# Optimization experiments

Hardware: AMD Instinct MI355X
Metric: run time of the kernel (lower is better)

The kernel has to match this reference:

```python
import jax, jax.numpy as jnp
import numpy as np

NUM_EMBEDDINGS = 4096
CODE_DIM = 256
NUM_CODEBOOKS = 4
COMMITMENT_COST = 0.25
CODEBOOK_COST = 1.0
EPS = 1e-10


def setup_inputs() -> dict:
    key = jax.random.key(0)
    k1, k2 = jax.random.split(key)
    z_bt = jax.random.normal(k1, (8192, NUM_CODEBOOKS * CODE_DIM), dtype=jnp.float32)
    # codebook init: uniform(-1/K, 1/K) as in the torch module
    embed = jax.random.uniform(k2, (NUM_EMBEDDINGS, CODE_DIM), dtype=jnp.float32,
                               minval=-1.0 / NUM_EMBEDDINGS, maxval=1.0 / NUM_EMBEDDINGS)
    return {"z_bt": z_bt, "embed": embed}


def reference(z_bt, embed):
    K, D = embed.shape            # [num_embeddings, code_dim]
    flat_z = z_bt.reshape(-1, D)  # [N*num_codebooks, code_dim]
    # squared-distance matrix: ||z||^2 - 2 z.e + ||e||^2
    distances = (jnp.sum(flat_z * flat_z, axis=1, keepdims=True)
                 - 2.0 * (flat_z @ embed.T)
                 + jnp.sum(embed * embed, axis=1)[None, :])  # [M, K]
    flat_indices = jnp.argmin(distances, axis=1)              # [M]
    quantized_bt = embed[flat_indices].reshape(z_bt.shape)    # [N, latent_dim]

    # use_ema=True, eval mode: codebook_loss is zero, no EMA buffer update
    codebook_loss = jnp.zeros((), dtype=z_bt.dtype)
    commitment_loss = jnp.mean((jax.lax.stop_gradient(quantized_bt) - z_bt) ** 2)
    loss = CODEBOOK_COST * codebook_loss + COMMITMENT_COST * commitment_loss

    # straight-through estimator
    quantized_st = z_bt + jax.lax.stop_gradient(quantized_bt - z_bt)

    # perplexity via histogram (same math as one_hot.mean(0))
    M = flat_indices.shape[0]
    counts = jnp.zeros((K,), dtype=z_bt.dtype).at[flat_indices].add(1.0)
    avg_probs = counts / M
    perplexity = jnp.exp(-jnp.sum(avg_probs * jnp.log(avg_probs + EPS)))

    indices = flat_indices.reshape(-1, NUM_CODEBOOKS)
    return quantized_st, indices, loss, codebook_loss, commitment_loss, perplexity
```

## Files before the change

kernel.cpp:

```cpp
#include <hip/hip_runtime.h>


constexpr int D_CODE  = 256;
constexpr int M_ROWS  = 32768;
constexpr int K_EMB   = 4096;
constexpr long Q_ELEMS = 8388608L;

constexpr size_t OFF_SUMZ = 0;
constexpr size_t OFF_SUME = 131072;
constexpr size_t OFF_PART = 147456;
constexpr size_t OFF_IDX  = 1196032;
constexpr size_t OFF_HIST = 1327104;
constexpr size_t OFF_DACC = 1343488;
constexpr size_t ZERO_LEN = 16392;

__device__ __forceinline__ float comp4(const float4& v, int kr) {
  return kr == 0 ? v.x : (kr == 1 ? v.y : (kr == 2 ? v.z : v.w));
}
__device__ __forceinline__ unsigned long long umin64(unsigned long long a, unsigned long long b) {
  return a < b ? a : b;
}

__global__ __launch_bounds__(256) void k_rowsums(const float* __restrict__ z,
                                                 const float* __restrict__ emb,
                                                 float* __restrict__ sumz,
                                                 float* __restrict__ sume) {
  int w = threadIdx.x >> 6, lane = threadIdx.x & 63;
  int row = blockIdx.x * 4 + w;
  const float* src;
  float* dst;
  if (row < M_ROWS) { src = z + (size_t)row * D_CODE; dst = sumz + row; }
  else              { src = emb + (size_t)(row - M_ROWS) * D_CODE; dst = sume + (row - M_ROWS); }
  float4 v = *(const float4*)(src + lane * 4);
  float s = (v.x * v.x + v.y * v.y) + (v.z * v.z + v.w * v.w);
  #pragma unroll
  for (int off = 32; off; off >>= 1) s += __shfl_xor(s, off, 64);
  if (lane == 0) *dst = s;
}


#define LOADT(ST, KK)                                                                       \
  _Pragma("unroll")                                                                         \
  for (int p = 0; p < 4; ++p) {                                                             \
    int g = 4 * tid + p;                                                                    \
    ST[p] = *(const float4*)(emb + (size_t)(c0 + (g >> 3)) * D_CODE + (KK) * 32 + (g & 7) * 4); \
  }

#define STORET(ST)                                                                          \
  _Pragma("unroll")                                                                         \
  for (int p = 0; p < 4; ++p) {                                                             \
    int g = 4 * tid + p;                                                                    \
    int cc = g >> 3, kq = g & 7;                                                            \
    float* wp = ebuf + (size_t)(4 * kq) * 132 + cc;                                         \
    wp[0 * 132] = ST[p].x;                                                                  \
    wp[1 * 132] = ST[p].y;                                                                  \
    wp[2 * 132] = ST[p].z;                                                                  \
    wp[3 * 132] = ST[p].w;                                                                  \
  }

#define COMPUTE(KK)                                                                         \
  _Pragma("unroll 1")                                                                       \
  for (int kq = 0; kq < 8; ++kq) {                                                          \
    float4 zf[8];                                                                           \
    _Pragma("unroll")                                                                       \
    for (int i = 0; i < 8; ++i)                                                             \
      zf[i] = *(const float4*)(zb + (size_t)i * D_CODE + (KK) * 32 + kq * 4);               \
    const float* ebase = ebuf + (size_t)(4 * kq) * 132 + tx * 4;                            \
    _Pragma("unroll")                                                                       \
    for (int kr = 0; kr < 4; ++kr) {                                                        \
      _Pragma("unroll")                                                                     \
      for (int g4 = 0; g4 < 4; ++g4) {                                                      \
        float4 ef = *(const float4*)(ebase + kr * 132 + g4 * 32);                           \
        _Pragma("unroll")                                                                   \
        for (int i = 0; i < 8; ++i) {                                                       \
          float zs = comp4(zf[i], kr);                                                      \
          acc[i][4 * g4 + 0] = fmaf(zs, ef.x, acc[i][4 * g4 + 0]);                          \
          acc[i][4 * g4 + 1] = fmaf(zs, ef.y, acc[i][4 * g4 + 1]);                          \
          acc[i][4 * g4 + 2] = fmaf(zs, ef.z, acc[i][4 * g4 + 2]);                          \
          acc[i][4 * g4 + 3] = fmaf(zs, ef.w, acc[i][4 * g4 + 3]);                          \
        }                                                                                   \
      }                                                                                     \
    }                                                                                       \
  }

__global__ __launch_bounds__(256, 2) void k_argmin(const float* __restrict__ z,
                                                   const float* __restrict__ emb,
                                                   const float* __restrict__ sumz,
                                                   const float* __restrict__ sume,
                                                   unsigned long long* __restrict__ partial) {
  __shared__ float ebuf[32 * 132];
  __shared__ unsigned long long red[256][8];

  const int tid = threadIdx.x;
  const int tx = tid & 7;
  const int ty = tid >> 3;
  const int rt = blockIdx.x >> 2;
  const int q  = blockIdx.x & 3;
  const int row0 = rt * 256;
  const int c00 = q * 1024;

  const float* zb = z + (size_t)(row0 + ty * 8) * D_CODE;

  unsigned long long best[8];
  #pragma unroll
  for (int i = 0; i < 8; ++i) best[i] = ~0ULL;

  for (int et = 0; et < 8; ++et) {
    const int c0 = c00 + et * 128;
    float acc[8][16];
    #pragma unroll
    for (int i = 0; i < 8; ++i)
      #pragma unroll
      for (int j = 0; j < 16; ++j) acc[i][j] = 0.0f;

    float4 stA[4], stB[4];
    LOADT(stA, 0)

    #pragma unroll 1
    for (int kk2 = 0; kk2 < 4; ++kk2) {
      __syncthreads();
      STORET(stA)
      LOADT(stB, 2 * kk2 + 1)
      __syncthreads();
      COMPUTE(2 * kk2)
      __syncthreads();
      STORET(stB)
      if (kk2 < 3) { LOADT(stA, 2 * kk2 + 2) }
      __syncthreads();
      COMPUTE(2 * kk2 + 1)
    }

    #pragma unroll
    for (int g4 = 0; g4 < 4; ++g4) {
      #pragma unroll
      for (int l = 0; l < 4; ++l) {
        int j = 4 * g4 + l;
        int cg = c0 + g4 * 32 + tx * 4 + l;
        float se = sume[cg];
        #pragma unroll
        for (int i = 0; i < 8; ++i) {
          float sz = sumz[row0 + ty * 8 + i];
          float dd = (sz - 2.0f * acc[i][j]) + se;
          unsigned long long key =
              ((unsigned long long)__float_as_uint(dd) << 32) | (unsigned int)cg;
          best[i] = umin64(best[i], key);
        }
      }
    }
  }

  #pragma unroll
  for (int i = 0; i < 8; ++i) red[ty * 8 + i][tx] = best[i];
  __syncthreads();
  {
    int r = tid;
    unsigned long long b = red[r][0];
    #pragma unroll
    for (int t = 1; t < 8; ++t) b = umin64(b, red[r][t]);
    partial[(size_t)q * M_ROWS + row0 + r] = b;
  }
}

__global__ __launch_bounds__(256) void k_merge(const unsigned long long* __restrict__ partial,
                                               int* __restrict__ idx,
                                               float* __restrict__ outI,
                                               unsigned int* __restrict__ hist) {
  int r = blockIdx.x * 256 + threadIdx.x;
  unsigned long long b = partial[r];
  b = umin64(b, partial[(size_t)M_ROWS + r]);
  b = umin64(b, partial[2 * (size_t)M_ROWS + r]);
  b = umin64(b, partial[3 * (size_t)M_ROWS + r]);
  int id = (int)(unsigned int)(b & 0xffffffffULL);
  idx[r] = id;
  outI[r] = (float)id;
  atomicAdd(&hist[id], 1u);
}

__global__ __launch_bounds__(256) void k_quant(const float* __restrict__ z,
                                               const float* __restrict__ emb,
                                               const int* __restrict__ idx,
                                               float* __restrict__ outQ,
                                               double* __restrict__ dacc) {
  __shared__ double sd[256];
  const long NF4 = Q_ELEMS / 4;
  long f0 = (long)blockIdx.x * 256 + threadIdx.x;
  double s = 0.0;
  for (long f = f0; f < NF4; f += 524288) {
    long m = f >> 6;
    int d4 = (int)(f & 63) * 4;
    int id = idx[m];
    float4 zv = *(const float4*)(z + f * 4);
    float4 qv = *(const float4*)(emb + (size_t)id * D_CODE + d4);
    float dx = qv.x - zv.x, dy = qv.y - zv.y, dz = qv.z - zv.z, dw = qv.w - zv.w;
    float4 ov;
    ov.x = zv.x + dx; ov.y = zv.y + dy; ov.z = zv.z + dz; ov.w = zv.w + dw;
    *(float4*)(outQ + f * 4) = ov;
    s += (double)dx * (double)dx + (double)dy * (double)dy
       + (double)dz * (double)dz + (double)dw * (double)dw;
  }
  sd[threadIdx.x] = s;
  __syncthreads();
  #pragma unroll
  for (int o = 128; o; o >>= 1) {
    if (threadIdx.x < o) sd[threadIdx.x] += sd[threadIdx.x + o];
    __syncthreads();
  }
  if (threadIdx.x == 0) atomicAdd(dacc, sd[0]);
}

__global__ __launch_bounds__(256) void k_final(const unsigned int* __restrict__ hist,
                                               const double* __restrict__ dacc,
                                               float* __restrict__ outS) {
  __shared__ double sd[256];
  double s = 0.0;
  for (int c = threadIdx.x; c < K_EMB; c += 256) {
    double p = (double)hist[c] * (1.0 / 32768.0);
    s += p * log(p + 1e-10);
  }
  sd[threadIdx.x] = s;
  __syncthreads();
  #pragma unroll
  for (int o = 128; o; o >>= 1) {
    if (threadIdx.x < o) sd[threadIdx.x] += sd[threadIdx.x + o];
    __syncthreads();
  }
  if (threadIdx.x == 0) {
    float commit = (float)(dacc[0] / (double)Q_ELEMS);
    outS[0] = 0.25f * commit;
    outS[1] = 0.0f;
    outS[2] = commit;
    outS[3] = (float)exp(-sd[0]);
  }
}

extern "C" void kernel_launch(void* const* d_in, const int* in_sizes, int n_in,
                              void* d_out, int out_size, void* d_ws, size_t ws_size,
                              hipStream_t stream) {
  const float* z   = (const float*)d_in[0];
  const float* emb = (const float*)d_in[1];
  float* out = (float*)d_out;
  char* ws = (char*)d_ws;

  float* sumz = (float*)(ws + OFF_SUMZ);
  float* sume = (float*)(ws + OFF_SUME);
  unsigned long long* partial = (unsigned long long*)(ws + OFF_PART);
  int* idx = (int*)(ws + OFF_IDX);
  unsigned int* hist = (unsigned int*)(ws + OFF_HIST);
  double* dacc = (double*)(ws + OFF_DACC);

  hipMemsetAsync(ws + OFF_HIST, 0, ZERO_LEN, stream);

  k_rowsums<<<9216, 256, 0, stream>>>(z, emb, sumz, sume);
  k_argmin<<<512, 256, 0, stream>>>(z, emb, sumz, sume, partial);
  k_merge<<<M_ROWS / 256, 256, 0, stream>>>(partial, idx, out + Q_ELEMS, hist);
  k_quant<<<2048, 256, 0, stream>>>(z, emb, idx, out, dacc);
  k_final<<<1, 256, 0, stream>>>(hist, dacc, out + Q_ELEMS + M_ROWS);
}
```

Baseline: 953.0 us.

## Restructure argmin GEMM with packed FMA, smaller codeword tiles and atomicMin merge

Rewrites the distance/argmin kernel. Each block now stages 32 codewords by 256 dims in shared memory and walks the full depth. Accumulation uses packed 2-wide float FMAs (v2f) and z rows are read directly from global memory. The grid doubles to 1024 blocks with 8 column splits, and per-row minima are combined via shuffles and a 64-bit atomicMin into a 0xFF-initialised buffer instead of partial arrays. The intent is higher occupancy and packed-FMA throughput, at the cost of less register reuse per tile, more global z traffic, and a shared-memory load and two block barriers for every 32-codeword tile.

```diff
diff --git a/kernel.cpp b/kernel.cpp
--- a/kernel.cpp
+++ b/kernel.cpp
@@ -6,17 +6,16 @@
 constexpr int K_EMB   = 4096;
 constexpr long Q_ELEMS = 8388608L;
 
+typedef float v2f __attribute__((ext_vector_type(2)));
+
 constexpr size_t OFF_SUMZ = 0;
 constexpr size_t OFF_SUME = 131072;
-constexpr size_t OFF_PART = 147456;
-constexpr size_t OFF_IDX  = 1196032;
-constexpr size_t OFF_HIST = 1327104;
-constexpr size_t OFF_DACC = 1343488;
+constexpr size_t OFF_BEST = 147456;
+constexpr size_t OFF_IDX  = 409600;
+constexpr size_t OFF_HIST = 540672;
+constexpr size_t OFF_DACC = 557056;
 constexpr size_t ZERO_LEN = 16392;
 
-__device__ __forceinline__ float comp4(const float4& v, int kr) {
-  return kr == 0 ? v.x : (kr == 1 ? v.y : (kr == 2 ? v.z : v.w));
-}
 __device__ __forceinline__ unsigned long long umin64(unsigned long long a, unsigned long long b) {
   return a < b ? a : b;
 }
@@ -38,138 +37,105 @@
   if (lane == 0) *dst = s;
 }
 
-
-#define LOADT(ST, KK)                                                                       \
-  _Pragma("unroll")                                                                         \
-  for (int p = 0; p < 4; ++p) {                                                             \
-    int g = 4 * tid + p;                                                                    \
-    ST[p] = *(const float4*)(emb + (size_t)(c0 + (g >> 3)) * D_CODE + (KK) * 32 + (g & 7) * 4); \
-  }
-
-#define STORET(ST)                                                                          \
-  _Pragma("unroll")                                                                         \
-  for (int p = 0; p < 4; ++p) {                                                             \
-    int g = 4 * tid + p;                                                                    \
-    int cc = g >> 3, kq = g & 7;                                                            \
-    float* wp = ebuf + (size_t)(4 * kq) * 132 + cc;                                         \
-    wp[0 * 132] = ST[p].x;                                                                  \
-    wp[1 * 132] = ST[p].y;                                                                  \
-    wp[2 * 132] = ST[p].z;                                                                  \
-    wp[3 * 132] = ST[p].w;                                                                  \
-  }
-
-#define COMPUTE(KK)                                                                         \
-  _Pragma("unroll 1")                                                                       \
-  for (int kq = 0; kq < 8; ++kq) {                                                          \
-    float4 zf[8];                                                                           \
-    _Pragma("unroll")                                                                       \
-    for (int i = 0; i < 8; ++i)                                                             \
-      zf[i] = *(const float4*)(zb + (size_t)i * D_CODE + (KK) * 32 + kq * 4);               \
-    const float* ebase = ebuf + (size_t)(4 * kq) * 132 + tx * 4;                            \
-    _Pragma("unroll")                                                                       \
-    for (int kr = 0; kr < 4; ++kr) {                                                        \
-      _Pragma("unroll")                                                                     \
-      for (int g4 = 0; g4 < 4; ++g4) {                                                      \
-        float4 ef = *(const float4*)(ebase + kr * 132 + g4 * 32);                           \
-        _Pragma("unroll")                                                                   \
-        for (int i = 0; i < 8; ++i) {                                                       \
-          float zs = comp4(zf[i], kr);                                                      \
-          acc[i][4 * g4 + 0] = fmaf(zs, ef.x, acc[i][4 * g4 + 0]);                          \
-          acc[i][4 * g4 + 1] = fmaf(zs, ef.y, acc[i][4 * g4 + 1]);                          \
-          acc[i][4 * g4 + 2] = fmaf(zs, ef.z, acc[i][4 * g4 + 2]);                          \
-          acc[i][4 * g4 + 3] = fmaf(zs, ef.w, acc[i][4 * g4 + 3]);                          \
-        }                                                                                   \
-      }                                                                                     \
-    }                                                                                       \
-  }
-
-__global__ __launch_bounds__(256, 2) void k_argmin(const float* __restrict__ z,
+__global__ __launch_bounds__(256, 4) void k_argmin(const float* __restrict__ z,
                                                    const float* __restrict__ emb,
                                                    const float* __restrict__ sumz,
                                                    const float* __restrict__ sume,
-                                                   unsigned long long* __restrict__ partial) {
-  __shared__ float ebuf[32 * 132];
-  __shared__ unsigned long long red[256][8];
+                                                   unsigned long long* __restrict__ best64) {
+  __shared__ float ebuf[32][260];
 
   const int tid = threadIdx.x;
   const int tx = tid & 7;
   const int ty = tid >> 3;
-  const int rt = blockIdx.x >> 2;
-  const int q  = blockIdx.x & 3;
+  const int rt = blockIdx.x >> 3;
+  const int q  = blockIdx.x & 7;
   const int row0 = rt * 256;
-  const int c00 = q * 1024;
-
-  const float* zb = z + (size_t)(row0 + ty * 8) * D_CODE;
-
-  unsigned long long best[8];
-  #pragma unroll
-  for (int i = 0; i < 8; ++i) best[i] = ~0ULL;
-
-  for (int et = 0; et < 8; ++et) {
-    const int c0 = c00 + et * 128;
-    float acc[8][16];
+  const int c00 = q * 512;
+
+  const float* zb = z + ((size_t)row0 + (size_t)ty * 8) * D_CODE;
+
+  float sz[8];
+  #pragma unroll
+  for (int i = 0; i < 8; ++i) sz[i] = sumz[row0 + ty * 8 + i];
+
+  const int scc = tid & 31;
+  const int sch = tid >> 5;
+
+  #pragma unroll 1
+  for (int et = 0; et < 16; ++et) {
+    const int c0 = c00 + et * 32;
+
+    __syncthreads();
+    {
+      const float* src = emb + (size_t)(c0 + scc) * D_CODE + sch * 32;
+      float* dst = &ebuf[scc][sch * 32];
+      #pragma unroll
+      for (int w = 0; w < 8; ++w)
+        *(float4*)(dst + w * 4) = *(const float4*)(src + w * 4);
+    }
+    __syncthreads();
+
+    v2f acc[8][4];
     #pragma unroll
     for (int i = 0; i < 8; ++i)
       #pragma unroll
-      for (int j = 0; j < 16; ++j) acc[i][j] = 0.0f;
-
-    float4 stA[4], stB[4];
-    LOADT(stA, 0)
+      for (int j = 0; j < 4; ++j) acc[i][j] = (v2f)(0.0f);
 
     #pragma unroll 1
-    for (int kk2 = 0; kk2 < 4; ++kk2) {
-      __syncthreads();
-      STORET(stA)
-      LOADT(stB, 2 * kk2 + 1)
-      __syncthreads();
-      COMPUTE(2 * kk2)
-      __syncthreads();
-      STORET(stB)
-      if (kk2 < 3) { LOADT(stA, 2 * kk2 + 2) }
-      __syncthreads();
-      COMPUTE(2 * kk2 + 1)
-    }
-
-    #pragma unroll
-    for (int g4 = 0; g4 < 4; ++g4) {
-      #pragma unroll
-      for (int l = 0; l < 4; ++l) {
-        int j = 4 * g4 + l;
-        int cg = c0 + g4 * 32 + tx * 4 + l;
-        float se = sume[cg];
+    for (int kc = 0; kc < 64; ++kc) {
+      v2f e0[4], e1[4];
+      #pragma unroll
+      for (int j = 0; j < 4; ++j) {
+        float4 ev = *(const float4*)&ebuf[j * 8 + tx][kc * 4];
+        e0[j] = (v2f){ev.x, ev.y};
+        e1[j] = (v2f){ev.z, ev.w};
+      }
+      #pragma unroll
+      for (int i = 0; i < 8; ++i) {
+        float4 zv = *(const float4*)(zb + (size_t)i * D_CODE + kc * 4);
+        v2f za = (v2f){zv.x, zv.y};
+        v2f zc = (v2f){zv.z, zv.w};
         #pragma unroll
-        for (int i = 0; i < 8; ++i) {
-          float sz = sumz[row0 + ty * 8 + i];
-          float dd = (sz - 2.0f * acc[i][j]) + se;
-          unsigned long long key =
-              ((unsigned long long)__float_as_uint(dd) << 32) | (unsigned int)cg;
-          best[i] = umin64(best[i], key);
+        for (int j = 0; j < 4; ++j) {
+          acc[i][j] = __builtin_elementwise_fma(za, e0[j], acc[i][j]);
+          acc[i][j] = __builtin_elementwise_fma(zc, e1[j], acc[i][j]);
         }
       }
     }
-  }
-
-  #pragma unroll
-  for (int i = 0; i < 8; ++i) red[ty * 8 + i][tx] = best[i];
-  __syncthreads();
-  {
-    int r = tid;
-    unsigned long long b = red[r][0];
-    #pragma unroll
-    for (int t = 1; t < 8; ++t) b = umin64(b, red[r][t]);
-    partial[(size_t)q * M_ROWS + row0 + r] = b;
-  }
-}
-
-__global__ __launch_bounds__(256) void k_merge(const unsigned long long* __restrict__ partial,
+
+    unsigned long long bestRow[8];
+    #pragma unroll
+    for (int i = 0; i < 8; ++i) bestRow[i] = ~0ULL;
+    #pragma unroll
+    for (int j = 0; j < 4; ++j) {
+      int cg = c0 + j * 8 + tx;
+      float se = sume[cg];
+      #pragma unroll
+      for (int i = 0; i < 8; ++i) {
+        float dot = acc[i][j].x + acc[i][j].y;
+        float dd = (sz[i] - 2.0f * dot) + se;
+        unsigned long long key =
+            ((unsigned long long)__float_as_uint(dd) << 32) | (unsigned int)cg;
+        bestRow[i] = umin64(bestRow[i], key);
+      }
+    }
+    #pragma unroll
+    for (int i = 0; i < 8; ++i) {
+      unsigned long long b = bestRow[i];
+      b = umin64(b, __shfl_xor(b, 1, 8));
+      b = umin64(b, __shfl_xor(b, 2, 8));
+      b = umin64(b, __shfl_xor(b, 4, 8));
+      if (tx == 0) atomicMin(&best64[row0 + ty * 8 + i], b);
+    }
+  }
+}
+
+__global__ __launch_bounds__(256) void k_merge(const unsigned long long* __restrict__ best64,
                                                int* __restrict__ idx,
                                                float* __restrict__ outI,
                                                unsigned int* __restrict__ hist) {
   int r = blockIdx.x * 256 + threadIdx.x;
-  unsigned long long b = partial[r];
-  b = umin64(b, partial[(size_t)M_ROWS + r]);
-  b = umin64(b, partial[2 * (size_t)M_ROWS + r]);
-  b = umin64(b, partial[3 * (size_t)M_ROWS + r]);
+  unsigned long long b = best64[r];
   int id = (int)(unsigned int)(b & 0xffffffffULL);
   idx[r] = id;
   outI[r] = (float)id;
@@ -243,16 +209,17 @@
 
   float* sumz = (float*)(ws + OFF_SUMZ);
   float* sume = (float*)(ws + OFF_SUME);
-  unsigned long long* partial = (unsigned long long*)(ws + OFF_PART);
+  unsigned long long* best64 = (unsigned long long*)(ws + OFF_BEST);
   int* idx = (int*)(ws + OFF_IDX);
   unsigned int* hist = (unsigned int*)(ws + OFF_HIST);
   double* dacc = (double*)(ws + OFF_DACC);
 
   hipMemsetAsync(ws + OFF_HIST, 0, ZERO_LEN, stream);
+  hipMemsetAsync(ws + OFF_BEST, 0xFF, 262144, stream);
 
   k_rowsums<<<9216, 256, 0, stream>>>(z, emb, sumz, sume);
-  k_argmin<<<512, 256, 0, stream>>>(z, emb, sumz, sume, partial);
-  k_merge<<<M_ROWS / 256, 256, 0, stream>>>(partial, idx, out + Q_ELEMS, hist);
+  k_argmin<<<1024, 256, 0, stream>>>(z, emb, sumz, sume, best64);
+  k_merge<<<M_ROWS / 256, 256, 0, stream>>>(best64, idx, out + Q_ELEMS, hist);
   k_quant<<<2048, 256, 0, stream>>>(z, emb, idx, out, dacc);
   k_final<<<1, 256, 0, stream>>>(hist, dacc, out + Q_ELEMS + M_ROWS);
 }
```

After: 3.027 ms. 218% more time.
